# Performance work log

Hardware: AMD Instinct MI355X
Metric: run time of the kernel (lower is better)

Reference implementation:

```python
import jax, jax.numpy as jnp
import numpy as np

T = 2048
HID = 4096
H = 32
HKV = 8
D = 128
EPS = 1e-5
THETA = 1e6
WINDOW = 1024


def setup_inputs() -> dict:
    key = jax.random.key(0)
    k1, k2, k3 = jax.random.split(key, 3)
    return {
        "positions": jnp.arange(T, dtype=jnp.int32),
        "hidden_states": jax.random.normal(k1, (T, HID), dtype=jnp.float32),
        "w_qkv": jax.random.normal(k2, (HID, (H + 2 * HKV) * D), dtype=jnp.float32) * 0.02,
        "q_norm_w": jnp.ones((D,), dtype=jnp.float32),
        "k_norm_w": jnp.ones((D,), dtype=jnp.float32),
        "w_o": jax.random.normal(k3, (H * D, HID), dtype=jnp.float32) * 0.02,
    }


def _rmsnorm(x, w):
    # per-head RMSNorm over last dim (head_dim)
    var = jnp.mean(x * x, axis=-1, keepdims=True)
    return x * jax.lax.rsqrt(var + EPS) * w


def _rope_neox(x, positions):
    # x: [T, heads, D]; neox style: rotate halves
    half = D // 2
    inv_freq = 1.0 / (THETA ** (jnp.arange(0, half, dtype=jnp.float32) / half))
    ang = positions.astype(jnp.float32)[:, None] * inv_freq  # [T, half]
    cos = jnp.cos(ang)[:, None, :]
    sin = jnp.sin(ang)[:, None, :]
    x1, x2 = x[..., :half], x[..., half:]
    return jnp.concatenate([x1 * cos - x2 * sin, x2 * cos + x1 * sin], axis=-1)


def reference(positions, hidden_states, w_qkv, q_norm_w, k_norm_w, w_o):
    qkv = hidden_states @ w_qkv  # [T, (H+2Hkv)*D]
    q, k, v = jnp.split(qkv, [H * D, (H + HKV) * D], axis=-1)
    q = _rmsnorm(q.reshape(T, H, D), q_norm_w)
    k = _rmsnorm(k.reshape(T, HKV, D), k_norm_w)
    v = v.reshape(T, HKV, D)

    q = _rope_neox(q, positions)
    k = _rope_neox(k, positions)

    # GQA: expand kv heads to H
    rep = H // HKV
    k = jnp.repeat(k, rep, axis=1)  # [T, H, D]
    v = jnp.repeat(v, rep, axis=1)

    scale = D ** -0.5
    scores = jnp.einsum('thd,shd->hts', q, k) * scale  # [H, T, T]
    i = jnp.arange(T)[:, None]
    j = jnp.arange(T)[None, :]
    mask = (j <= i) & (i - j < WINDOW)  # causal + sliding window
    scores = jnp.where(mask[None], scores, -jnp.inf)
    probs = jax.nn.softmax(scores, axis=-1)
    attn = jnp.einsum('hts,shd->thd', probs, v).reshape(T, H * D)
    return attn @ w_o
```

## Files before the change

kernel.cpp:

```cpp
#include <hip/hip_runtime.h>
#include <hip/hip_bf16.h>
#include <stdint.h>

#define T_SEQ  2048
#define HIDDEN 4096
#define NHEAD  32
#define NKV    8
#define HDIM   128
#define NQKV   6144
#define WINDOW 1024
#define SCALE  0.08838834764831845f
#define SHIFT  12.0f

typedef __attribute__((ext_vector_type(8))) short          short8;
typedef __attribute__((ext_vector_type(8))) unsigned short ushort8_t;
typedef __attribute__((ext_vector_type(4))) float          floatx4;

__device__ __forceinline__ unsigned short f2bf(float f) {
    union { float f; unsigned int u; } v; v.f = f;
    unsigned int u = v.u;
    unsigned int r = (u + 0x7FFFu + ((u >> 16) & 1u)) >> 16;
    return (unsigned short)r;
}
__device__ __forceinline__ float bf2f(unsigned short u) {
    union { unsigned int u; float f; } v; v.u = ((unsigned int)u) << 16;
    return v.f;
}

#define GLOBAL_AS(p) ((const __attribute__((address_space(1))) void*)(p))
#define LDS_AS(p)    ((__attribute__((address_space(3))) void*)(p))

#define S_BARRIER() do { asm volatile("" ::: "memory");  \
                         __builtin_amdgcn_s_barrier();   \
                         asm volatile("" ::: "memory"); } while (0)

__global__ __launch_bounds__(256) void convert_bf16_kernel(
        const float* __restrict__ X, unsigned short* __restrict__ Y, int n4) {
    int i = blockIdx.x * blockDim.x + threadIdx.x;
    if (i < n4) {
        float4 v = ((const float4*)X)[i];
        ushort4 o;
        o.x = f2bf(v.x); o.y = f2bf(v.y); o.z = f2bf(v.z); o.w = f2bf(v.w);
        ((ushort4*)Y)[i] = o;
    }
}

__global__ __launch_bounds__(256) void transpose_bf16_kernel(
        const float* __restrict__ W, unsigned short* __restrict__ Wt, int K, int N) {
    __shared__ float tile[128][33];
    const int n0 = blockIdx.x * 32, k0 = blockIdx.y * 128;
    const int tid = threadIdx.x;
    const int rr = tid >> 3, cc = tid & 7;
    #pragma unroll
    for (int p = 0; p < 4; ++p) {
        int r = p * 32 + rr;
        float4 v = *(const float4*)&W[(size_t)(k0 + r) * N + n0 + cc * 4];
        tile[r][cc * 4 + 0] = v.x; tile[r][cc * 4 + 1] = v.y;
        tile[r][cc * 4 + 2] = v.z; tile[r][cc * 4 + 3] = v.w;
    }
    __syncthreads();
    const int nL = tid >> 3, kc = tid & 7;
    #pragma unroll
    for (int q = 0; q < 2; ++q) {
        int kbase = kc * 8 + q * 64;
        ushort8_t o;
        #pragma unroll
        for (int j = 0; j < 8; ++j) o[j] = f2bf(tile[kbase + j][nL]);
        *(ushort8_t*)&Wt[(size_t)(n0 + nL) * K + k0 + kbase] = o;
    }
}

#define STG3_A(bufi, kt, r)                                                       \
    __builtin_amdgcn_global_load_lds(                                             \
        GLOBAL_AS(A + (size_t)(m0 + rRow[r]) * K + ((kt) << 6) + rOff[r]),        \
        LDS_AS(&As3[bufi][((r) * 256 + tid) * 8]), 16, 0, 0)
#define STG3_B(bufi, kt, r)                                                       \
    __builtin_amdgcn_global_load_lds(                                             \
        GLOBAL_AS(B + (size_t)(n0 + rRow[r]) * K + ((kt) << 6) + rOff[r]),        \
        LDS_AS(&Bs3[bufi][((r) * 256 + tid) * 8]), 16, 0, 0)

template <bool BF16_OUT>
__global__ __launch_bounds__(256, 2) void gemm_bt3_kernel(
        const unsigned short* __restrict__ A,
        const unsigned short* __restrict__ B,
        void* __restrict__ Cv, int M, int N, int K) {
    __shared__ __align__(16) unsigned short As3[2][128 * 64];
    __shared__ __align__(16) unsigned short Bs3[2][128 * 64];

    const int tid  = threadIdx.x;
    const int lane = tid & 63, wave = tid >> 6;
    const int wr = wave >> 1, wc = wave & 1;
    const int lrow = lane & 15, hi = lane >> 4;

    const int nwg = gridDim.x * gridDim.y;
    int wg = blockIdx.y * gridDim.x + blockIdx.x;
    wg = (wg & 7) * (nwg >> 3) + (wg >> 3);
    const int bx = wg % gridDim.x;
    const int by = wg / gridDim.x;
    const int m0 = by * 128, n0 = bx * 128;

    const int NT = K >> 6;

    int rRow[4], rOff[4];
    #pragma unroll
    for (int r = 0; r < 4; ++r) {
        int idx = r * 256 + tid;
        int row = idx >> 3;
        rRow[r] = row;
        rOff[r] = ((idx & 7) ^ (row & 7)) * 8;
    }

    const int sA0   = (hi ^ (lrow & 7)) * 8;
    const int aBase = (wr * 64 + lrow) * 64;
    const int bBase = (wc * 64 + lrow) * 64;

    floatx4 acc[4][4] = {};

    auto compute_tile = [&](int cur) {
        const unsigned short* ap = &As3[cur][0];
        const unsigned short* bp = &Bs3[cur][0];
        short8 af[4][2], bf[4][2];
        #pragma unroll
        for (int m = 0; m < 4; ++m)
            #pragma unroll
            for (int kh = 0; kh < 2; ++kh)
                af[m][kh] = *(const short8*)(ap + aBase + m * 1024 + (sA0 ^ (kh << 5)));
        #pragma unroll
        for (int n = 0; n < 4; ++n)
            #pragma unroll
            for (int kh = 0; kh < 2; ++kh)
                bf[n][kh] = *(const short8*)(bp + bBase + n * 1024 + (sA0 ^ (kh << 5)));
        __builtin_amdgcn_s_setprio(1);
        #pragma unroll
        for (int m = 0; m < 4; ++m)
            #pragma unroll
            for (int n = 0; n < 4; ++n) {
                acc[m][n] = __builtin_amdgcn_mfma_f32_16x16x32_bf16(
                    af[m][0], bf[n][0], acc[m][n], 0, 0, 0);
                acc[m][n] = __builtin_amdgcn_mfma_f32_16x16x32_bf16(
                    af[m][1], bf[n][1], acc[m][n], 0, 0, 0);
            }
        __builtin_amdgcn_s_setprio(0);
    };

    #pragma unroll
    for (int r = 0; r < 4; ++r) STG3_A(0, 0, r);
    #pragma unroll
    for (int r = 0; r < 4; ++r) STG3_B(0, 0, r);
    asm volatile("s_waitcnt vmcnt(0)" ::: "memory");
    S_BARRIER();

    for (int t = 0; t < NT - 1; ++t) {
        const int cur = t & 1;
        #pragma unroll
        for (int r = 0; r < 4; ++r) STG3_A(cur ^ 1, t + 1, r);
        #pragma unroll
        for (int r = 0; r < 4; ++r) STG3_B(cur ^ 1, t + 1, r);
        compute_tile(cur);
        asm volatile("s_waitcnt vmcnt(0)" ::: "memory");
        S_BARRIER();
    }
    compute_tile((NT - 1) & 1);

    const int rowb = hi * 4, col = lrow;
    #pragma unroll
    for (int mi = 0; mi < 4; ++mi)
        #pragma unroll
        for (int ni = 0; ni < 4; ++ni) {
            size_t base = (size_t)(m0 + wr * 64 + mi * 16 + rowb) * N
                        + (n0 + wc * 64 + ni * 16 + col);
            #pragma unroll
            for (int r = 0; r < 4; ++r) {
                if (BF16_OUT)
                    ((unsigned short*)Cv)[base + (size_t)r * N] = f2bf(acc[mi][ni][r]);
                else
                    ((float*)Cv)[base + (size_t)r * N] = acc[mi][ni][r];
            }
        }
}

__global__ __launch_bounds__(256) void rope_table_kernel(
        const int* __restrict__ positions, float2* __restrict__ rope) {
    int idx = blockIdx.x * 256 + threadIdx.x;
    int t = idx >> 6, i = idx & 63;
    float inv_freq = expf((float)i * -0.2158673524681918f);
    float sn, cs;
    sincosf((float)positions[t] * inv_freq, &sn, &cs);
    rope[idx] = make_float2(cs, sn);
}

__global__ __launch_bounds__(256) void qkv_post_kernel(
        const unsigned short* __restrict__ qkv, const float2* __restrict__ rope,
        const float* __restrict__ qw, const float* __restrict__ kw,
        unsigned short* __restrict__ qb,
        unsigned short* __restrict__ kb,
        unsigned short* __restrict__ vbT) {
    const int head = blockIdx.y;
    const int t0   = blockIdx.x * 32;
    const int tid  = threadIdx.x;

    if (head < 40) {
        const int r  = tid >> 3;
        const int q8 = tid & 7;
        const int t  = t0 + r;
        const unsigned short* src = qkv + (size_t)t * NQKV
                         + (head < 32 ? head * 128 : 4096 + (head - 32) * 128)
                         + q8 * 16;
        const float* w = (head < 32) ? qw : kw;

        ushort8_t u0 = *(const ushort8_t*)src;
        ushort8_t u1 = *(const ushort8_t*)(src + 8);
        float x[16];
        #pragma unroll
        for (int j = 0; j < 8; ++j) { x[j] = bf2f(u0[j]); x[8 + j] = bf2f(u1[j]); }

        float ss = 0.f;
        #pragma unroll
        for (int j = 0; j < 16; ++j) ss = fmaf(x[j], x[j], ss);
        ss += __shfl_xor(ss, 1); ss += __shfl_xor(ss, 2); ss += __shfl_xor(ss, 4);
        float sc = rsqrtf(ss * (1.f / 128.f) + 1e-5f);

        float xn[16], xp[16];
        #pragma unroll
        for (int j = 0; j < 16; ++j) xn[j] = x[j] * sc * w[q8 * 16 + j];
        #pragma unroll
        for (int j = 0; j < 16; ++j) xp[j] = __shfl_xor(xn[j], 4);

        const float2* rp = rope + (size_t)t * 64 + (q8 & 3) * 16;
        ushort8_t o0, o1;
        #pragma unroll
        for (int j = 0; j < 8; ++j) {
            float2 cs = rp[j];
            float res = (q8 < 4) ? (xn[j] * cs.x - xp[j] * cs.y)
                                 : (xn[j] * cs.x + xp[j] * cs.y);
            o0[j] = f2bf(res);
        }
        #pragma unroll
        for (int j = 0; j < 8; ++j) {
            float2 cs = rp[8 + j];
            float res = (q8 < 4) ? (xn[8+j] * cs.x - xp[8+j] * cs.y)
                                 : (xn[8+j] * cs.x + xp[8+j] * cs.y);
            o1[j] = f2bf(res);
        }
        unsigned short* dst = (head < 32)
            ? qb + ((size_t)t * 32 + head) * 128 + q8 * 16
            : kb + ((size_t)t * 8 + (head - 32)) * 128 + q8 * 16;
        *(ushort8_t*)dst       = o0;
        *(ushort8_t*)(dst + 8) = o1;
    } else {
        __shared__ float tile[128][33];
        const int hk = head - 40;
        {
            const int r = tid >> 3, c8 = tid & 7;
            const unsigned short* src =
                qkv + (size_t)(t0 + r) * NQKV + 5120 + hk * 128 + c8 * 16;
            ushort8_t u0 = *(const ushort8_t*)src;
            ushort8_t u1 = *(const ushort8_t*)(src + 8);
            #pragma unroll
            for (int j = 0; j < 8; ++j) {
                tile[c8 * 16 + j][r]     = bf2f(u0[j]);
                tile[c8 * 16 + 8 + j][r] = bf2f(u1[j]);
            }
        }
        __syncthreads();
        {
            const int d = tid >> 1, th = tid & 1;
            ushort8_t o0, o1;
            #pragma unroll
            for (int j = 0; j < 8; ++j) o0[j] = f2bf(tile[d][th * 16 + j]);
            #pragma unroll
            for (int j = 0; j < 8; ++j) o1[j] = f2bf(tile[d][th * 16 + 8 + j]);
            unsigned short* dst = vbT + ((size_t)hk * 128 + d) * T_SEQ + t0 + th * 16;
            *(ushort8_t*)dst       = o0;
            *(ushort8_t*)(dst + 8) = o1;
        }
    }
}

__global__ __launch_bounds__(256) void attention_kernel(
        const unsigned short* __restrict__ qb,
        const unsigned short* __restrict__ kb,
        const unsigned short* __restrict__ vbT,
        unsigned short* __restrict__ attnb) {
    const int h    = blockIdx.x & 31;
    const int Q0   = (blockIdx.x >> 5) * 64;
    const int tid  = threadIdx.x, wave = tid >> 6, lane = tid & 63;
    const int keyA = lane & 15, g = lane >> 4;
    const int hk   = h >> 2;
    const int qlo  = Q0 + wave * 16;

    __shared__ __align__(16) unsigned short ks [32 * 128];
    __shared__ __align__(16) unsigned short vsT[128 * 32];
    __shared__ __align__(16) unsigned short Pa [4 * 16 * 40];

    unsigned short* pw = Pa + wave * 640;

    short8 qa[4];
    {
        const unsigned short* qp = qb + ((size_t)(qlo + keyA) * 32 + h) * 128 + g * 8;
        #pragma unroll
        for (int s = 0; s < 4; ++s) qa[s] = *(const short8*)(qp + s * 32);
    }

    floatx4 acc[8] = {};
    float l_part[4] = {0.f, 0.f, 0.f, 0.f};

    const int s_begin = (Q0 >= WINDOW) ? ((Q0 - (WINDOW - 1)) & ~31) : 0;
    const int s_end   = Q0 + 63;

    for (int s0 = s_begin; s0 <= s_end; s0 += 32) {
        #pragma unroll
        for (int i = 0; i < 2; ++i) {
            int c = i * 256 + tid;
            {   int row = c >> 4, u = c & 15, su = u ^ (row & 7);
                const unsigned short* kp = kb + ((size_t)(s0 + row) * 8 + hk) * 128 + su * 8;
                __builtin_amdgcn_global_load_lds(GLOBAL_AS(kp), LDS_AS(ks + c * 8), 16, 0, 0); }
            {   int d = c >> 2, u = c & 3, su = u ^ (d & 3);
                const unsigned short* vp = vbT + ((size_t)hk * 128 + d) * T_SEQ + s0 + su * 8;
                __builtin_amdgcn_global_load_lds(GLOBAL_AS(vp), LDS_AS(vsT + c * 8), 16, 0, 0); }
        }
        __syncthreads();

        if (s0 <= qlo + 15 && s0 + 31 >= qlo - (WINDOW - 1)) {
            floatx4 sa0 = {}, sa1 = {};
            #pragma unroll
            for (int kst = 0; kst < 4; ++kst) {
                int u = g + 4 * kst;
                short8 k0 = *(const short8*)(ks + keyA * 128 + (u ^ (keyA & 7)) * 8);
                short8 k1 = *(const short8*)(ks + (16 + keyA) * 128 + (u ^ ((16 + keyA) & 7)) * 8);
                sa0 = __builtin_amdgcn_mfma_f32_16x16x32_bf16(qa[kst], k0, sa0, 0, 0, 0);
                sa1 = __builtin_amdgcn_mfma_f32_16x16x32_bf16(qa[kst], k1, sa1, 0, 0, 0);
            }
            float p0[4], p1[4];
            #pragma unroll
            for (int r = 0; r < 4; ++r) {
                int row = qlo + 4 * g + r;
                int sA = s0 + keyA, sB = sA + 16;
                bool vA = (sA <= row) && (row - sA < WINDOW);
                bool vB = (sB <= row) && (row - sB < WINDOW);
                p0[r] = vA ? __expf(fmaf(sa0[r], SCALE, -SHIFT)) : 0.f;
                p1[r] = vB ? __expf(fmaf(sa1[r], SCALE, -SHIFT)) : 0.f;
                l_part[r] += p0[r] + p1[r];
            }
            #pragma unroll
            for (int r = 0; r < 4; ++r) {
                pw[(4 * g + r) * 40 + keyA]      = f2bf(p0[r]);
                pw[(4 * g + r) * 40 + keyA + 16] = f2bf(p1[r]);
            }
            short8 pf = *(const short8*)(pw + keyA * 40 + g * 8);

            #pragma unroll
            for (int t = 0; t < 8; ++t) {
                int d = t * 16 + keyA;
                short8 vf = *(const short8*)(vsT + d * 32 + (g ^ (d & 3)) * 8);
                acc[t] = __builtin_amdgcn_mfma_f32_16x16x32_bf16(pf, vf, acc[t], 0, 0, 0);
            }
        }
        __syncthreads();
    }

    float inv[4];
    #pragma unroll
    for (int r = 0; r < 4; ++r) {
        float l = l_part[r];
        l += __shfl_xor(l, 1); l += __shfl_xor(l, 2);
        l += __shfl_xor(l, 4); l += __shfl_xor(l, 8);
        inv[r] = 1.f / l;
    }
    #pragma unroll
    for (int t = 0; t < 8; ++t)
        #pragma unroll
        for (int r = 0; r < 4; ++r)
            attnb[(size_t)(qlo + 4 * g + r) * 4096 + h * 128 + t * 16 + keyA] =
                f2bf(acc[t][r] * inv[r]);
}

extern "C" void kernel_launch(void* const* d_in, const int* in_sizes, int n_in,
                              void* d_out, int out_size, void* d_ws, size_t ws_size,
                              hipStream_t stream) {
    const int*   positions = (const int*)  d_in[0];
    const float* hs        = (const float*)d_in[1];
    const float* w_qkv     = (const float*)d_in[2];
    const float* q_norm_w  = (const float*)d_in[3];
    const float* k_norm_w  = (const float*)d_in[4];
    const float* w_o       = (const float*)d_in[5];
    float* out = (float*)d_out;

    char* ws = (char*)d_ws;
    unsigned short* hsb   = (unsigned short*)(ws);
    unsigned short* wqkvt = (unsigned short*)(ws + (size_t)(16u << 20));
    unsigned short* wot   = (unsigned short*)(ws + (size_t)(64u << 20));
    unsigned short* qkvb  = (unsigned short*)(ws + (size_t)(96u << 20));
    unsigned short* qb    = (unsigned short*)(ws + (size_t)(16u << 20));
    unsigned short* kb    = (unsigned short*)(ws + (size_t)(32u << 20));
    unsigned short* vbT   = (unsigned short*)(ws + (size_t)(36u << 20));
    float2*         rope  = (float2*)        (ws + (size_t)(40u << 20));
    unsigned short* attnb = hsb;

    convert_bf16_kernel<<<dim3((T_SEQ * HIDDEN / 4 + 255) / 256), 256, 0, stream>>>(
        hs, hsb, T_SEQ * HIDDEN / 4);
    transpose_bf16_kernel<<<dim3(NQKV / 32, HIDDEN / 128), 256, 0, stream>>>(
        w_qkv, wqkvt, HIDDEN, NQKV);
    transpose_bf16_kernel<<<dim3(HIDDEN / 32, HIDDEN / 128), 256, 0, stream>>>(
        w_o, wot, HIDDEN, HIDDEN);
    gemm_bt3_kernel<true><<<dim3(NQKV / 128, T_SEQ / 128), 256, 0, stream>>>(
        hsb, wqkvt, qkvb, T_SEQ, NQKV, HIDDEN);
    rope_table_kernel<<<dim3(T_SEQ * 64 / 256), 256, 0, stream>>>(positions, rope);
    qkv_post_kernel<<<dim3(T_SEQ / 32, 48), 256, 0, stream>>>(
        qkvb, rope, q_norm_w, k_norm_w, qb, kb, vbT);
    attention_kernel<<<dim3((T_SEQ / 64) * NHEAD), 256, 0, stream>>>(
        qb, kb, vbT, attnb);
    gemm_bt3_kernel<false><<<dim3(HIDDEN / 128, T_SEQ / 128), 256, 0, stream>>>(
        attnb, wot, out, T_SEQ, HIDDEN, HIDDEN);
}
```

Measured before the change: 552.6 us.

## Use 128x192 tiled GEMM with XCD-aware block remap for QKV projection

Adds a new GEMM kernel for the QKV projection that uses 128x192 output tiles (each wave computes 64x96) and remaps workgroup IDs so that neighbouring tiles are grouped across the eight chiplets. The larger N tile raises MFMA work per LDS load, and the remap is meant to improve L2 reuse of shared A/B rows. The 6144-wide N dimension divides evenly into 32 tiles, giving 512 workgroups. In exchange the kernel uses more registers and more LDS, which may lower occupancy; the launch bound requests two blocks per CU.

```diff
diff --git a/kernel.cpp b/kernel.cpp
--- a/kernel.cpp
+++ b/kernel.cpp
@@ -169,6 +169,123 @@
         for (int ni = 0; ni < 4; ++ni) {
             size_t base = (size_t)(m0 + wr * 64 + mi * 16 + rowb) * N
                         + (n0 + wc * 64 + ni * 16 + col);
+            #pragma unroll
+            for (int r = 0; r < 4; ++r) {
+                if (BF16_OUT)
+                    ((unsigned short*)Cv)[base + (size_t)r * N] = f2bf(acc[mi][ni][r]);
+                else
+                    ((float*)Cv)[base + (size_t)r * N] = acc[mi][ni][r];
+            }
+        }
+}
+
+#define STG4_A(bufi, kt, r)                                                       \
+    __builtin_amdgcn_global_load_lds(                                             \
+        GLOBAL_AS(A + (size_t)(m0 + rRowA[r]) * K + ((kt) << 6) + rOffA[r]),      \
+        LDS_AS(&As4[bufi][((r) * 256 + tid) * 8]), 16, 0, 0)
+#define STG4_B(bufi, kt, r)                                                       \
+    __builtin_amdgcn_global_load_lds(                                             \
+        GLOBAL_AS(B + (size_t)(n0 + rRowB[r]) * K + ((kt) << 6) + rOffB[r]),      \
+        LDS_AS(&Bs4[bufi][((r) * 256 + tid) * 8]), 16, 0, 0)
+
+template <bool BF16_OUT>
+__global__ __launch_bounds__(256, 2) void gemm_bt4_kernel(
+        const unsigned short* __restrict__ A,
+        const unsigned short* __restrict__ B,
+        void* __restrict__ Cv, int M, int N, int K) {
+    __shared__ __align__(16) unsigned short As4[2][128 * 64];
+    __shared__ __align__(16) unsigned short Bs4[2][192 * 64];
+
+    const int tid  = threadIdx.x;
+    const int lane = tid & 63, wave = tid >> 6;
+    const int wr = wave >> 1, wc = wave & 1;
+    const int lrow = lane & 15, hi = lane >> 4;
+
+    const int nwg = gridDim.x * gridDim.y;
+    int wg = blockIdx.y * gridDim.x + blockIdx.x;
+    wg = (wg & 7) * (nwg >> 3) + (wg >> 3);
+    const int by = wg % gridDim.x;
+    const int bx = wg / gridDim.x;
+    const int m0 = by * 128, n0 = bx * 192;
+
+    const int NT = K >> 6;
+
+    int rRowA[4], rOffA[4];
+    #pragma unroll
+    for (int r = 0; r < 4; ++r) {
+        int idx = r * 256 + tid;
+        int row = idx >> 3;
+        rRowA[r] = row;
+        rOffA[r] = ((idx & 7) ^ (row & 7)) * 8;
+    }
+    int rRowB[6], rOffB[6];
+    #pragma unroll
+    for (int r = 0; r < 6; ++r) {
+        int idx = r * 256 + tid;
+        int row = idx >> 3;
+        rRowB[r] = row;
+        rOffB[r] = ((idx & 7) ^ (row & 7)) * 8;
+    }
+
+    const int sA0   = (hi ^ (lrow & 7)) * 8;
+    const int aBase = (wr * 64 + lrow) * 64;
+    const int bBase = (wc * 96 + lrow) * 64;
+
+    floatx4 acc[4][6] = {};
+
+    auto compute_tile = [&](int cur) {
+        const unsigned short* ap = &As4[cur][0];
+        const unsigned short* bp = &Bs4[cur][0];
+        short8 af[4][2], bf[6][2];
+        #pragma unroll
+        for (int m = 0; m < 4; ++m)
+            #pragma unroll
+            for (int kh = 0; kh < 2; ++kh)
+                af[m][kh] = *(const short8*)(ap + aBase + m * 1024 + (sA0 ^ (kh << 5)));
+        #pragma unroll
+        for (int n = 0; n < 6; ++n)
+            #pragma unroll
+            for (int kh = 0; kh < 2; ++kh)
+                bf[n][kh] = *(const short8*)(bp + bBase + n * 1024 + (sA0 ^ (kh << 5)));
+        __builtin_amdgcn_s_setprio(1);
+        #pragma unroll
+        for (int m = 0; m < 4; ++m)
+            #pragma unroll
+            for (int n = 0; n < 6; ++n) {
+                acc[m][n] = __builtin_amdgcn_mfma_f32_16x16x32_bf16(
+                    af[m][0], bf[n][0], acc[m][n], 0, 0, 0);
+                acc[m][n] = __builtin_amdgcn_mfma_f32_16x16x32_bf16(
+                    af[m][1], bf[n][1], acc[m][n], 0, 0, 0);
+            }
+        __builtin_amdgcn_s_setprio(0);
+    };
+
+    #pragma unroll
+    for (int r = 0; r < 4; ++r) STG4_A(0, 0, r);
+    #pragma unroll
+    for (int r = 0; r < 6; ++r) STG4_B(0, 0, r);
+    asm volatile("s_waitcnt vmcnt(0)" ::: "memory");
+    S_BARRIER();
+
+    for (int t = 0; t < NT - 1; ++t) {
+        const int cur = t & 1;
+        #pragma unroll
+        for (int r = 0; r < 4; ++r) STG4_A(cur ^ 1, t + 1, r);
+        #pragma unroll
+        for (int r = 0; r < 6; ++r) STG4_B(cur ^ 1, t + 1, r);
+        compute_tile(cur);
+        asm volatile("s_waitcnt vmcnt(0)" ::: "memory");
+        S_BARRIER();
+    }
+    compute_tile((NT - 1) & 1);
+
+    const int rowb = hi * 4, col = lrow;
+    #pragma unroll
+    for (int mi = 0; mi < 4; ++mi)
+        #pragma unroll
+        for (int ni = 0; ni < 6; ++ni) {
+            size_t base = (size_t)(m0 + wr * 64 + mi * 16 + rowb) * N
+                        + (n0 + wc * 96 + ni * 16 + col);
             #pragma unroll
             for (int r = 0; r < 4; ++r) {
                 if (BF16_OUT)
@@ -403,7 +520,7 @@
         w_qkv, wqkvt, HIDDEN, NQKV);
     transpose_bf16_kernel<<<dim3(HIDDEN / 32, HIDDEN / 128), 256, 0, stream>>>(
         w_o, wot, HIDDEN, HIDDEN);
-    gemm_bt3_kernel<true><<<dim3(NQKV / 128, T_SEQ / 128), 256, 0, stream>>>(
+    gemm_bt4_kernel<true><<<dim3(T_SEQ / 128, NQKV / 192), 256, 0, stream>>>(
         hsb, wqkvt, qkvb, T_SEQ, NQKV, HIDDEN);
     rope_table_kernel<<<dim3(T_SEQ * 64 / 256), 256, 0, stream>>>(positions, rope);
     qkv_post_kernel<<<dim3(T_SEQ / 32, 48), 256, 0, stream>>>(
```

Result: faster. 504.2 us (-8.8%).
